# Kernel tuning notes

Measured on AMD Instinct MI355X. Metric: run time of the kernel, lower is better.

Reference implementation:

```python
import jax, jax.numpy as jnp
import numpy as np

B, C, H, W = 16, 21, 512, 512


def setup_inputs() -> dict:
    key = jax.random.key(0)
    k1, k2 = jax.random.split(key)
    # y_pred: class probabilities (softmax over class dim of random logits)
    logits = jax.random.normal(k1, (B, C, H, W), dtype=jnp.float32)
    y_pred = jax.nn.softmax(logits, axis=1)
    # y_true: one-hot ground truth built from random integer labels
    labels = jax.random.randint(k2, (B, H, W), 0, C)
    y_true = jax.nn.one_hot(labels, C, axis=1, dtype=jnp.float32)  # [B,C,H,W]
    return {"y_pred": y_pred, "y_true": y_true, "bg": 0}


def reference(y_pred, y_true, bg):
    eps = 1e-11
    # static slice: classes l in [bg, C)
    yt = y_true[:, bg:]  # [B, C', H, W]
    yp = y_pred[:, bg:]
    ta = jnp.sum(yt, axis=(2, 3))            # [B, C'] target mass per class
    tb = jnp.sum(yp, axis=(2, 3))            # [B, C'] pred mass per class
    inter = jnp.sum(yt * yp, axis=(2, 3))    # [B, C'] intersection
    valid = ta != 0                          # classes skipped when target empty
    dice = jnp.where(valid, 2.0 * inter / (ta + tb + eps), 0.0)
    cpt2 = jnp.sum(valid, axis=1).astype(jnp.float32)  # [B] non-empty classes
    denom = cpt2 - bg                        # matches original cpt2 - bg divisor
    batch_valid = denom != 0
    safe_denom = jnp.where(batch_valid, denom, 1.0)
    tmp = jnp.where(batch_valid, jnp.sum(dice, axis=1) / safe_denom, 0.0)  # [B]
    cpt1 = jnp.sum(batch_valid).astype(jnp.float32)
    loss = 1.0 - jnp.sum(tmp) / jnp.maximum(cpt1, 1.0)
    return jnp.where(cpt1 > 0, loss, jnp.float32(-1.0))
```

## Files before the change

### kernel.cpp

```cpp
#include <hip/hip_runtime.h>


#define BB 16
#define CC 21
#define HW (512 * 512)
#define SPLIT 64
#define CHUNK (HW / SPLIT)
#define NBC (BB * CC)

__global__ void zero_ws_kernel(float* __restrict__ ws, int n) {
    int i = blockIdx.x * blockDim.x + threadIdx.x;
    if (i < n) ws[i] = 0.0f;
}

__global__ __launch_bounds__(256) void dice_reduce_kernel(
    const float* __restrict__ y_pred,
    const float* __restrict__ y_true,
    const int* __restrict__ bg_ptr,
    float* __restrict__ ws)
{
    const int blk   = blockIdx.x;
    const int split = blk % SPLIT;
    const int bc    = blk / SPLIT;
    const int c     = bc % CC;
    const int bg    = *bg_ptr;
    if (c < bg) return;

    const size_t base = (size_t)bc * HW + (size_t)split * CHUNK;
    const float4* __restrict__ p4 = (const float4*)(y_pred + base);
    const float4* __restrict__ t4 = (const float4*)(y_true + base);

    float st = 0.0f, sp = 0.0f, stp = 0.0f;
    const int tid = threadIdx.x;

    #pragma unroll
    for (int i = tid; i < CHUNK / 4; i += 256) {
        float4 p = p4[i];
        float4 t = t4[i];
        sp  += (p.x + p.y) + (p.z + p.w);
        st  += (t.x + t.y) + (t.z + t.w);
        stp += (t.x * p.x + t.y * p.y) + (t.z * p.z + t.w * p.w);
    }

    #pragma unroll
    for (int off = 32; off > 0; off >>= 1) {
        st  += __shfl_down(st,  off, 64);
        sp  += __shfl_down(sp,  off, 64);
        stp += __shfl_down(stp, off, 64);
    }

    __shared__ float sm[3][4];
    const int wave = tid >> 6;
    const int lane = tid & 63;
    if (lane == 0) { sm[0][wave] = st; sm[1][wave] = sp; sm[2][wave] = stp; }
    __syncthreads();

    if (tid == 0) {
        float a  = (sm[0][0] + sm[0][1]) + (sm[0][2] + sm[0][3]);
        float b  = (sm[1][0] + sm[1][1]) + (sm[1][2] + sm[1][3]);
        float ab = (sm[2][0] + sm[2][1]) + (sm[2][2] + sm[2][3]);
        atomicAdd(&ws[3 * bc + 0], a);
        atomicAdd(&ws[3 * bc + 1], b);
        atomicAdd(&ws[3 * bc + 2], ab);
    }
}

__global__ __launch_bounds__(256) void dice_final_kernel(
    const float* __restrict__ ws,
    const int* __restrict__ bg_ptr,
    float* __restrict__ out)
{
    const float eps = 1e-11f;
    const int bg = *bg_ptr;
    __shared__ float dice_sum[BB];
    __shared__ int   valid_cnt[BB];

    const int tid = threadIdx.x;
    if (tid < BB) { dice_sum[tid] = 0.0f; valid_cnt[tid] = 0; }
    __syncthreads();

    for (int i = tid; i < NBC; i += blockDim.x) {
        int c = i % CC;
        int b = i / CC;
        if (c < bg) continue;
        float ta    = ws[3 * i + 0];
        float tb    = ws[3 * i + 1];
        float inter = ws[3 * i + 2];
        if (ta != 0.0f) {
            float dice = 2.0f * inter / (ta + tb + eps);
            atomicAdd(&dice_sum[b], dice);
            atomicAdd(&valid_cnt[b], 1);
        }
    }
    __syncthreads();

    if (tid == 0) {
        float sum_tmp = 0.0f;
        int cpt1 = 0;
        for (int b = 0; b < BB; b++) {
            float denom = (float)valid_cnt[b] - (float)bg;
            if (denom != 0.0f) {
                sum_tmp += dice_sum[b] / denom;
                cpt1++;
            }
        }
        float loss = 1.0f - sum_tmp / fmaxf((float)cpt1, 1.0f);
        out[0] = (cpt1 > 0) ? loss : -1.0f;
    }
}

extern "C" void kernel_launch(void* const* d_in, const int* in_sizes, int n_in,
                              void* d_out, int out_size, void* d_ws, size_t ws_size,
                              hipStream_t stream) {
    const float* y_pred = (const float*)d_in[0];
    const float* y_true = (const float*)d_in[1];
    const int*   bg_ptr = (const int*)d_in[2];
    float* out = (float*)d_out;
    float* ws  = (float*)d_ws;

    const int nws = 3 * NBC;
    zero_ws_kernel<<<(nws + 255) / 256, 256, 0, stream>>>(ws, nws);

    dice_reduce_kernel<<<NBC * SPLIT, 256, 0, stream>>>(y_pred, y_true, bg_ptr, ws);

    dice_final_kernel<<<1, 256, 0, stream>>>(ws, bg_ptr, out);
}
```

Before: 663.8 us.

## Replace atomic accumulation with per-block partials, drop zero kernel, use nontemporal loads

Each reduction block now writes its three partial sums to its own slot instead of issuing atomics, so the workspace-zeroing kernel is removed and one launch is saved. The final kernel sums the partials over 16 splits per (batch, class), with one thread per pair. SPLIT drops from 64 to 16, giving fewer and longer blocks, and loads use nontemporal hints with partial unrolling. The risks are lower parallelism from fewer blocks (5376) and a larger workspace requirement.

```diff
diff --git a/kernel.cpp b/kernel.cpp
--- a/kernel.cpp
+++ b/kernel.cpp
@@ -4,20 +4,18 @@
 #define BB 16
 #define CC 21
 #define HW (512 * 512)
-#define SPLIT 64
+#define SPLIT 16
 #define CHUNK (HW / SPLIT)
 #define NBC (BB * CC)
+#define NPART (NBC * SPLIT)
 
-__global__ void zero_ws_kernel(float* __restrict__ ws, int n) {
-    int i = blockIdx.x * blockDim.x + threadIdx.x;
-    if (i < n) ws[i] = 0.0f;
-}
+typedef float floatx4 __attribute__((ext_vector_type(4)));
 
 __global__ __launch_bounds__(256) void dice_reduce_kernel(
     const float* __restrict__ y_pred,
     const float* __restrict__ y_true,
     const int* __restrict__ bg_ptr,
-    float* __restrict__ ws)
+    float* __restrict__ part)
 {
     const int blk   = blockIdx.x;
     const int split = blk % SPLIT;
@@ -27,16 +25,16 @@
     if (c < bg) return;
 
     const size_t base = (size_t)bc * HW + (size_t)split * CHUNK;
-    const float4* __restrict__ p4 = (const float4*)(y_pred + base);
-    const float4* __restrict__ t4 = (const float4*)(y_true + base);
+    const floatx4* __restrict__ p4 = (const floatx4*)(y_pred + base);
+    const floatx4* __restrict__ t4 = (const floatx4*)(y_true + base);
 
     float st = 0.0f, sp = 0.0f, stp = 0.0f;
     const int tid = threadIdx.x;
 
-    #pragma unroll
+    #pragma unroll 4
     for (int i = tid; i < CHUNK / 4; i += 256) {
-        float4 p = p4[i];
-        float4 t = t4[i];
+        floatx4 p = __builtin_nontemporal_load(&p4[i]);
+        floatx4 t = __builtin_nontemporal_load(&t4[i]);
         sp  += (p.x + p.y) + (p.z + p.w);
         st  += (t.x + t.y) + (t.z + t.w);
         stp += (t.x * p.x + t.y * p.y) + (t.z * p.z + t.w * p.w);
@@ -56,17 +54,14 @@
     __syncthreads();
 
     if (tid == 0) {
-        float a  = (sm[0][0] + sm[0][1]) + (sm[0][2] + sm[0][3]);
-        float b  = (sm[1][0] + sm[1][1]) + (sm[1][2] + sm[1][3]);
-        float ab = (sm[2][0] + sm[2][1]) + (sm[2][2] + sm[2][3]);
-        atomicAdd(&ws[3 * bc + 0], a);
-        atomicAdd(&ws[3 * bc + 1], b);
-        atomicAdd(&ws[3 * bc + 2], ab);
+        part[0 * NPART + blk] = (sm[0][0] + sm[0][1]) + (sm[0][2] + sm[0][3]);
+        part[1 * NPART + blk] = (sm[1][0] + sm[1][1]) + (sm[1][2] + sm[1][3]);
+        part[2 * NPART + blk] = (sm[2][0] + sm[2][1]) + (sm[2][2] + sm[2][3]);
     }
 }
 
-__global__ __launch_bounds__(256) void dice_final_kernel(
-    const float* __restrict__ ws,
+__global__ __launch_bounds__(384) void dice_final_kernel(
+    const float* __restrict__ part,
     const int* __restrict__ bg_ptr,
     float* __restrict__ out)
 {
@@ -79,17 +74,22 @@
     if (tid < BB) { dice_sum[tid] = 0.0f; valid_cnt[tid] = 0; }
     __syncthreads();
 
-    for (int i = tid; i < NBC; i += blockDim.x) {
-        int c = i % CC;
-        int b = i / CC;
-        if (c < bg) continue;
-        float ta    = ws[3 * i + 0];
-        float tb    = ws[3 * i + 1];
-        float inter = ws[3 * i + 2];
-        if (ta != 0.0f) {
-            float dice = 2.0f * inter / (ta + tb + eps);
-            atomicAdd(&dice_sum[b], dice);
-            atomicAdd(&valid_cnt[b], 1);
+    if (tid < NBC) {
+        const int c = tid % CC;
+        const int b = tid / CC;
+        if (c >= bg) {
+            float ta = 0.0f, tb = 0.0f, inter = 0.0f;
+            #pragma unroll
+            for (int s = 0; s < SPLIT; s++) {
+                ta    += part[0 * NPART + tid * SPLIT + s];
+                tb    += part[1 * NPART + tid * SPLIT + s];
+                inter += part[2 * NPART + tid * SPLIT + s];
+            }
+            if (ta != 0.0f) {
+                float dice = 2.0f * inter / (ta + tb + eps);
+                atomicAdd(&dice_sum[b], dice);
+                atomicAdd(&valid_cnt[b], 1);
+            }
         }
     }
     __syncthreads();
@@ -115,13 +115,9 @@
     const float* y_pred = (const float*)d_in[0];
     const float* y_true = (const float*)d_in[1];
     const int*   bg_ptr = (const int*)d_in[2];
-    float* out = (float*)d_out;
-    float* ws  = (float*)d_ws;
+    float* out  = (float*)d_out;
+    float* part = (float*)d_ws;
 
-    const int nws = 3 * NBC;
-    zero_ws_kernel<<<(nws + 255) / 256, 256, 0, stream>>>(ws, nws);
-
-    dice_reduce_kernel<<<NBC * SPLIT, 256, 0, stream>>>(y_pred, y_true, bg_ptr, ws);
-
-    dice_final_kernel<<<1, 256, 0, stream>>>(ws, bg_ptr, out);
+    dice_reduce_kernel<<<NBC * SPLIT, 256, 0, stream>>>(y_pred, y_true, bg_ptr, part);
+    dice_final_kernel<<<1, 384, 0, stream>>>(part, bg_ptr, out);
 }
```

Measured after the change: 611.1 us. 1.09x faster.
